# Kernel tuning notes

Measured on AMD Instinct MI355X. Metric: run time of the kernel, lower is better.

The kernel has to match this reference:

```python
import jax, jax.numpy as jnp
import numpy as np

B, N, D_ATOM, HID, L = 32, 64, 5, 256, 9
E = N * N
F_E = 2 * HID + 2  # [h_i, h_j, d^2, edge_attr]


def _gather(x, idx):
    # x: (B, N, D), idx: (B, E) -> (B, E, D)
    return jax.vmap(lambda a, i: a[i])(x, idx)


def _segsum(data, idx, n):
    # per-batch unsorted segment sum over destination node idx
    return jax.vmap(lambda d, i: jax.ops.segment_sum(d, i, num_segments=n))(data, idx)


def _safe_dist(diff):
    # sqrt of squared norm, safe at 0 (masked self-edges) for grads
    return jnp.sqrt(jnp.maximum(jnp.sum(diff ** 2, axis=-1, keepdims=True), 1e-12))


def _remove_mean(x, mask):
    n = jnp.sum(mask, axis=1, keepdims=True)
    return (x - jnp.sum(x, axis=1, keepdims=True) / n) * mask


def setup_inputs() -> dict:
    key = jax.random.key(0)
    ks = iter(jax.random.split(key, 32))

    def W(shape):
        return jax.random.normal(next(ks), shape, jnp.float32) * 0.02

    x_in = jax.random.normal(next(ks), (B, N, 3), jnp.float32)
    h_in = jax.random.uniform(next(ks), (B, N, D_ATOM), dtype=jnp.float32)
    t = jax.random.uniform(next(ks), (B, N, 1), dtype=jnp.float32)
    ii, jj = jnp.meshgrid(jnp.arange(N), jnp.arange(N), indexing='ij')
    edges = jnp.stack([ii.reshape(-1), jj.reshape(-1)], axis=-1).astype(jnp.int32)  # (E,2) all pairs
    edge_indices = jnp.broadcast_to(edges[None], (B, E, 2))
    node_mask = jnp.ones((B, N, 1), jnp.float32)
    em = (edges[:, 0] != edges[:, 1]).astype(jnp.float32)[:, None]  # mask self-edges
    edge_mask = jnp.broadcast_to(em[None], (B, E, 1))
    params = dict(
        win_w=W((D_ATOM + 1, HID)), win_b=jnp.zeros((HID,), jnp.float32),
        wout_w=W((HID, D_ATOM + 1)), wout_b=jnp.zeros((D_ATOM + 1,), jnp.float32),
        we_w1=W((L, F_E, HID)), we_b1=jnp.zeros((L, HID), jnp.float32),
        we_w2=W((L, HID, HID)), we_b2=jnp.zeros((L, HID), jnp.float32),
        attn_w=W((L, HID, 1)), attn_b=jnp.zeros((L, 1), jnp.float32),
        wh_w1=W((L, 2 * HID, HID)), wh_b1=jnp.zeros((L, HID), jnp.float32),
        wh_w2=W((L, HID, HID)), wh_b2=jnp.zeros((L, HID), jnp.float32),
        wx_w1=W((L, F_E, HID)), wx_b1=jnp.zeros((L, HID), jnp.float32),
        wx_w2=W((L, HID, HID)), wx_b2=jnp.zeros((L, HID), jnp.float32),
        wx_w3=W((L, HID, 1)),
    )
    return dict(x_in=x_in, h_in=h_in, t=t, node_mask=node_mask, edge_mask=edge_mask,
                edge_indices=edge_indices, **params)


def reference(x_in, h_in, t, node_mask, edge_mask, edge_indices,
              win_w, win_b, wout_w, wout_b,
              we_w1, we_b1, we_w2, we_b2, attn_w, attn_b,
              wh_w1, wh_b1, wh_w2, wh_b2,
              wx_w1, wx_b1, wx_w2, wx_b2, wx_w3):
    idx_i = edge_indices[..., 0]
    idx_j = edge_indices[..., 1]
    # fixed edge attribute: initial pairwise distance
    d_in = _safe_dist(_gather(x_in, idx_i) - _gather(x_in, idx_j)) * edge_mask
    h0 = jnp.concatenate([h_in, t], axis=-1) @ win_w + win_b

    def block(carry, p):
        x, h = carry
        ew1, eb1, ew2, eb2, aw, ab, hw1, hb1, hw2, hb2, xw1, xb1, xw2, xb2, xw3 = p
        diff = (_gather(x, idx_i) - _gather(x, idx_j)) * edge_mask  # (B,E,3)
        d = _safe_dist(diff)  # (B,E,1)
        feat = jnp.concatenate([_gather(h, idx_i), _gather(h, idx_j), d ** 2, d_in], axis=-1) * edge_mask
        # edge MLP + attention gate, aggregated to node i
        m = jax.nn.silu(jax.nn.silu(feat @ ew1 + eb1) @ ew2 + eb2)
        em_agg = _segsum(jax.nn.sigmoid(m @ aw + ab) * m, idx_i, N)
        h_new = (h + (jax.nn.silu(jnp.concatenate([h, em_agg], axis=-1) @ hw1 + hb1) @ hw2 + hb2)) * node_mask
        # coordinate update (no bias on last layer)
        s = jax.nn.silu(jax.nn.silu(feat @ xw1 + xb1) @ xw2 + xb2) @ xw3  # (B,E,1)
        x_new = (x + _segsum(diff / (d + 1.0) * s, idx_i, N)) * node_mask
        return (x_new, h_new), None

    stacked = (we_w1, we_b1, we_w2, we_b2, attn_w, attn_b,
               wh_w1, wh_b1, wh_w2, wh_b2, wx_w1, wx_b1, wx_w2, wx_b2, wx_w3)
    (x, h), _ = jax.lax.scan(block, (x_in, h0), stacked)
    x_out = _remove_mean((x - x_in) * node_mask, node_mask)
    h_out = ((h @ wout_w + wout_b) * node_mask)[..., :-1]
    return jnp.concatenate([x_out, h_out], axis=-1)
```

## Files before the change

### kernel.cpp

```cpp
#include <hip/hip_runtime.h>
#include <hip/hip_bf16.h>
#include <math.h>


#define NB   32
#define NN   64
#define EPB  4096
#define HID  256
#define NL   9

typedef __attribute__((ext_vector_type(8))) short bfrag;
typedef __attribute__((ext_vector_type(4))) float f32x4;
typedef __attribute__((ext_vector_type(2))) float f32x2;

__device__ __forceinline__ float fast_rcp(float x) { return __builtin_amdgcn_rcpf(x); }
__device__ __forceinline__ float silu_f(float x) { return x * fast_rcp(1.f + __expf(-x)); }
__device__ __forceinline__ float sigm_f(float x) { return fast_rcp(1.f + __expf(-x)); }
__device__ __forceinline__ ushort bf16rne(float x) {
    unsigned u = __builtin_bit_cast(unsigned, x);
    u = (u + 0x7fffu + ((u >> 16) & 1u)) >> 16;
    return (ushort)u;
}
__device__ __forceinline__ float bf16tof(ushort h) {
    unsigned u = ((unsigned)h) << 16;
    return __builtin_bit_cast(float, u);
}
__device__ __forceinline__ unsigned pk2(f32x2 v) {
    float2 f; f.x = v.x; f.y = v.y;
    __hip_bfloat162 t = __float22bfloat162_rn(f);
    unsigned u;
    __builtin_memcpy(&u, &t, 4);
    return u;
}
__device__ __forceinline__ f32x2 fma2(f32x2 a, f32x2 b, f32x2 c) {
    return __builtin_elementwise_fma(a, b, c);
}
__device__ __forceinline__ f32x4 fma4(f32x4 a, f32x4 b, f32x4 c) {
    return __builtin_elementwise_fma(a, b, c);
}
__device__ __forceinline__ f32x2 silu2(f32x2 v) {
    f32x2 e = { __expf(-v.x), __expf(-v.y) };
    f32x2 d = e + (f32x2){1.f, 1.f};
    f32x2 r = { fast_rcp(d.x), fast_rcp(d.y) };
    return v * r;
}
__device__ __forceinline__ f32x4 silu4(f32x4 v) {
    f32x4 e = { __expf(-v.x), __expf(-v.y), __expf(-v.z), __expf(-v.w) };
    f32x4 d = e + (f32x4){1.f, 1.f, 1.f, 1.f};
    f32x4 r = { fast_rcp(d.x), fast_rcp(d.y), fast_rcp(d.z), fast_rcp(d.w) };
    return v * r;
}

__global__ void edm_k0_pre(const float* __restrict__ x_in, const float* __restrict__ h_in,
                           const float* __restrict__ t_in,
                           const float* __restrict__ win_w, const float* __restrict__ win_b,
                           float* __restrict__ h0, float* __restrict__ din_ws,
                           float* __restrict__ x0)
{
    int blk = blockIdx.x, tid = threadIdx.x;
    if (blk < NB * NN) {
        int node = blk;
        float acc = win_b[tid];
        #pragma unroll
        for (int k = 0; k < 5; ++k) acc += h_in[node * 5 + k] * win_w[k * HID + tid];
        acc += t_in[node] * win_w[5 * HID + tid];
        h0[node * HID + tid] = acc;
    } else if (blk < NB * NN + 512) {
        int e = (blk - NB * NN) * 256 + tid;
        int b = e >> 12, r = e & 4095, i = r >> 6, j = r & 63;
        const float* xb = x_in + b * NN * 3;
        float d0 = xb[i*3+0] - xb[j*3+0];
        float d1 = xb[i*3+1] - xb[j*3+1];
        float d2 = xb[i*3+2] - xb[j*3+2];
        float ss = d0*d0 + d1*d1 + d2*d2;
        float d  = sqrtf(fmaxf(ss, 1e-12f));
        din_ws[e] = (i != j) ? d : 0.f;
    } else {
        int idx = (blk - (NB * NN + 512)) * 256 + tid;
        if (idx < NB * NN * 3) x0[idx] = x_in[idx];
    }
}

__global__ void edm_k5_prep(const float* __restrict__ we_w2, const float* __restrict__ wx_w2,
                            ushort* __restrict__ W2Te, ushort* __restrict__ W2Tx)
{
    __shared__ float t_s[64][65];
    int blk = blockIdx.x;
    int mat = blk / 144, rem = blk % 144, l = rem >> 4, tile = rem & 15;
    int kt = tile >> 2, nt = tile & 3;
    const float* src = (mat ? wx_w2 : we_w2) + l * HID * HID;
    ushort* dst = (mat ? W2Tx : W2Te) + l * HID * HID;
    int col = threadIdx.x & 63, rg = threadIdx.x >> 6;
    #pragma unroll
    for (int it = 0; it < 16; ++it) {
        int row = rg * 16 + it;
        t_s[row][col] = src[(kt * 64 + row) * HID + nt * 64 + col];
    }
    __syncthreads();
    #pragma unroll
    for (int it = 0; it < 16; ++it) {
        int n = rg * 16 + it;
        dst[(nt * 64 + n) * HID + kt * 64 + col] = bf16rne(t_s[col][n]);
    }
}

__global__ void edm_k5b_prep(const float* __restrict__ we_w1, const float* __restrict__ wx_w1,
                             ushort* __restrict__ W1Th, ushort* __restrict__ W1Tl)
{
    __shared__ float t_s[64][65];
    int blk = blockIdx.x;
    int tile = blk & 15, out = (blk >> 4) & 3, l = blk >> 6;
    int kt = tile >> 2, nt = tile & 3;
    const float* src = ((out >= 2) ? wx_w1 : we_w1) + l * 514 * HID + (out & 1) * 256 * HID;
    size_t doff = ((size_t)(l * 4 + out)) * HID * HID;
    ushort* dh = W1Th + doff;
    ushort* dl = W1Tl + doff;
    int col = threadIdx.x & 63, rg = threadIdx.x >> 6;
    #pragma unroll
    for (int it = 0; it < 16; ++it) {
        int row = rg * 16 + it;
        t_s[row][col] = src[(kt * 64 + row) * HID + nt * 64 + col];
    }
    __syncthreads();
    #pragma unroll
    for (int it = 0; it < 16; ++it) {
        int n = rg * 16 + it;
        float v = t_s[col][n];
        ushort h = bf16rne(v);
        float lo = v - bf16tof(h);
        dh[(nt * 64 + n) * HID + kt * 64 + col] = h;
        dl[(nt * 64 + n) * HID + kt * 64 + col] = bf16rne(lo);
    }
}

__global__ void edm_k5c_prep(const float* __restrict__ wh_w1, const float* __restrict__ wh_w2,
                             ushort* __restrict__ W3h, ushort* __restrict__ W3l,
                             ushort* __restrict__ W4h, ushort* __restrict__ W4l)
{
    __shared__ float t_s[64][65];
    int blk = blockIdx.x;
    const float* src; ushort* dh; ushort* dl; int kt, nt, Kdim;
    if (blk < 288) {
        int l = blk >> 5, tile = blk & 31;
        kt = tile >> 2; nt = tile & 3; Kdim = 512;
        src = wh_w1 + (size_t)l * 512 * HID;
        dh = W3h + (size_t)l * HID * 512;
        dl = W3l + (size_t)l * HID * 512;
    } else {
        int b2 = blk - 288;
        int l = b2 >> 4, tile = b2 & 15;
        kt = tile >> 2; nt = tile & 3; Kdim = 256;
        src = wh_w2 + (size_t)l * HID * HID;
        dh = W4h + (size_t)l * HID * HID;
        dl = W4l + (size_t)l * HID * HID;
    }
    int col = threadIdx.x & 63, rg = threadIdx.x >> 6;
    #pragma unroll
    for (int it = 0; it < 16; ++it) {
        int row = rg * 16 + it;
        t_s[row][col] = src[(size_t)(kt * 64 + row) * HID + nt * 64 + col];
    }
    __syncthreads();
    #pragma unroll
    for (int it = 0; it < 16; ++it) {
        int n = rg * 16 + it;
        float v = t_s[col][n];
        ushort h = bf16rne(v);
        float lo = v - bf16tof(h);
        dh[(size_t)(nt * 64 + n) * Kdim + kt * 64 + col] = h;
        dl[(size_t)(nt * 64 + n) * Kdim + kt * 64 + col] = bf16rne(lo);
    }
}

__global__ __launch_bounds__(256)
void edm_k1_mfma(const float* __restrict__ h,
                 const ushort* __restrict__ W1Th, const ushort* __restrict__ W1Tl,
                 const float* __restrict__ we_b1, const float* __restrict__ wx_b1,
                 const float* __restrict__ we_w2, const float* __restrict__ we_b2,
                 const float* __restrict__ attn_w, const float* __restrict__ attn_b,
                 float* __restrict__ HeA, float* __restrict__ HeB,
                 float* __restrict__ HxA, float* __restrict__ HxB,
                 float* __restrict__ self_em, int l)
{
    int tid = threadIdx.x;
    if (blockIdx.x == 512) {
        __shared__ float m1s[HID];
        __shared__ float ms[HID];
        __shared__ float wred[4];
        __shared__ float gsh;
        const float* eb1 = we_b1 + l * HID;
        m1s[tid] = silu_f(eb1[tid]);
        __syncthreads();
        const float* W2 = we_w2 + l * HID * HID;
        float acc = we_b2[l * HID + tid];
        for (int k = 0; k < HID; ++k) acc += m1s[k] * W2[k * HID + tid];
        float mv = silu_f(acc);
        ms[tid] = mv;
        float p = mv * attn_w[l * HID + tid];
        #pragma unroll
        for (int off = 32; off > 0; off >>= 1) p += __shfl_down(p, off, 64);
        if ((tid & 63) == 0) wred[tid >> 6] = p;
        __syncthreads();
        if (tid == 0) gsh = sigm_f(wred[0] + wred[1] + wred[2] + wred[3] + attn_b[l]);
        __syncthreads();
        self_em[tid] = gsh * ms[tid];
        return;
    }

    __shared__ __align__(16) ushort Ah_s[16384];
    __shared__ __align__(16) ushort Al_s[16384];

    const int cq = blockIdx.x & 3;
    const int out = (blockIdx.x >> 2) & 3;
    const int ntile = blockIdx.x >> 4;
    const int base = ntile * 64;

    {
        const int c  = tid & 31;
        const int jg = tid >> 5;
        const int k0 = c * 8;
        #pragma unroll
        for (int it = 0; it < 8; ++it) {
            int m = it * 8 + jg;
            f32x4 h0 = *(const f32x4*)&h[(base + m) * HID + k0];
            f32x4 h1 = *(const f32x4*)&h[(base + m) * HID + k0 + 4];
            uint4 phi, plo;
            {
                ushort ax = bf16rne(h0.x), ay = bf16rne(h0.y);
                phi.x = (unsigned)ax | ((unsigned)ay << 16);
                plo.x = pk2((f32x2){h0.x - bf16tof(ax), h0.y - bf16tof(ay)});
            }
            {
                ushort ax = bf16rne(h0.z), ay = bf16rne(h0.w);
                phi.y = (unsigned)ax | ((unsigned)ay << 16);
                plo.y = pk2((f32x2){h0.z - bf16tof(ax), h0.w - bf16tof(ay)});
            }
            {
                ushort ax = bf16rne(h1.x), ay = bf16rne(h1.y);
                phi.z = (unsigned)ax | ((unsigned)ay << 16);
                plo.z = pk2((f32x2){h1.x - bf16tof(ax), h1.y - bf16tof(ay)});
            }
            {
                ushort ax = bf16rne(h1.z), ay = bf16rne(h1.w);
                phi.w = (unsigned)ax | ((unsigned)ay << 16);
                plo.w = pk2((f32x2){h1.z - bf16tof(ax), h1.w - bf16tof(ay)});
            }
            unsigned off = (unsigned)(m * 256 + ((c ^ (m & 7)) * 8));
            *(uint4*)&Ah_s[off] = phi;
            *(uint4*)&Al_s[off] = plo;
        }
    }
    __syncthreads();

    const int w = tid >> 6, lane = tid & 63, quad = lane >> 4, l16 = lane & 15;
    const int col = cq * 64 + w * 16 + l16;
    const ushort* Bh = W1Th + ((size_t)(l * 4 + out)) * HID * HID + (size_t)col * HID;
    const ushort* Bl = W1Tl + ((size_t)(l * 4 + out)) * HID * HID + (size_t)col * HID;

    f32x4 acc[4];
    #pragma unroll
    for (int mt = 0; mt < 4; ++mt) acc[mt] = (f32x4){0.f, 0.f, 0.f, 0.f};

    #pragma unroll
    for (int kt = 0; kt < 8; ++kt) {
        const int kof = kt * 32 + quad * 8;
        const int ch  = (kt * 4 + quad) ^ (l16 & 7);
        bfrag bh = *(const bfrag*)&Bh[kof];
        bfrag bl = *(const bfrag*)&Bl[kof];
        bfrag ahr[4], alr[4];
        #pragma unroll
        for (int mt = 0; mt < 4; ++mt) {
            ahr[mt] = *(const bfrag*)&Ah_s[(mt * 16 + l16) * 256 + ch * 8];
            alr[mt] = *(const bfrag*)&Al_s[(mt * 16 + l16) * 256 + ch * 8];
        }
        #pragma unroll
        for (int mt = 0; mt < 4; ++mt) {
            acc[mt] = __builtin_amdgcn_mfma_f32_16x16x32_bf16(ahr[mt], bh, acc[mt], 0, 0, 0);
            acc[mt] = __builtin_amdgcn_mfma_f32_16x16x32_bf16(ahr[mt], bl, acc[mt], 0, 0, 0);
            acc[mt] = __builtin_amdgcn_mfma_f32_16x16x32_bf16(alr[mt], bh, acc[mt], 0, 0, 0);
        }
    }

    float bias = 0.f;
    if (out == 0) bias = we_b1[l * HID + col];
    else if (out == 2) bias = wx_b1[l * HID + col];
    float* dst = (out == 0) ? HeA : (out == 1) ? HeB : (out == 2) ? HxA : HxB;
    #pragma unroll
    for (int mt = 0; mt < 4; ++mt)
        #pragma unroll
        for (int r = 0; r < 4; ++r)
            dst[(base + mt * 16 + quad * 4 + r) * HID + col] = acc[mt][r] + bias;
}

__global__ __launch_bounds__(256, 4)
void edm_kb_gemm(const float* __restrict__ x_cur, float* __restrict__ x_next,
                 const float* __restrict__ HeA, const float* __restrict__ HeB,
                 const float* __restrict__ HxA, const float* __restrict__ HxB,
                 const float* __restrict__ din_ws,
                 const float* __restrict__ we_w1, const float* __restrict__ we_b1,
                 const float* __restrict__ wx_w1, const float* __restrict__ wx_b1,
                 const ushort* __restrict__ W2Te, const ushort* __restrict__ W2Tx,
                 const float* __restrict__ we_b2, const float* __restrict__ wx_b2,
                 const float* __restrict__ attn_w, const float* __restrict__ attn_b,
                 const float* __restrict__ wx_w3,
                 float* __restrict__ em_agg, int l)
{
    __shared__ __align__(16) ushort A_s[16384];
    __shared__ float red_s[256];
    __shared__ float sc_s[64];
    __shared__ float x_s[192];
    __shared__ float d2_s[64], din_s[64];

    const int tid = threadIdx.x;
    const int blk = blockIdx.x;
    const int p = blk >> 11, rem = blk & 2047;
    const int i = rem >> 5, b = rem & 31;
    const int bi = b * 64 + i;

    if (tid < 192) x_s[tid] = x_cur[b * 192 + tid];
    if (tid >= 192) {
        int j = tid - 192;
        float d0 = x_cur[b * 192 + i*3+0] - x_cur[b * 192 + j*3+0];
        float d1 = x_cur[b * 192 + i*3+1] - x_cur[b * 192 + j*3+1];
        float d2 = x_cur[b * 192 + i*3+2] - x_cur[b * 192 + j*3+2];
        float ss = d0*d0 + d1*d1 + d2*d2;
        float d  = sqrtf(fmaxf(ss, 1e-12f));
        d2_s[j]  = d * d;
        din_s[j] = din_ws[b * EPB + i * 64 + j];
    }
    __syncthreads();

    {
        const float* W1  = (p ? wx_w1 : we_w1) + l * 514 * HID;
        const float* HA  = (p ? HxA : HeA);
        const float* HB  = (p ? HxB : HeB);
        const float* b1p = (p ? wx_b1 : we_b1) + l * HID;

        const int c  = tid & 31;
        const int jg = tid >> 5;
        const int k0 = c * 8;

        f32x4 ra0 = *(const f32x4*)&HA[(b * 64 + i) * HID + k0];
        f32x4 ra1 = *(const f32x4*)&HA[(b * 64 + i) * HID + k0 + 4];
        f32x4 wa0 = *(const f32x4*)&W1[512 * HID + k0];
        f32x4 wa1 = *(const f32x4*)&W1[512 * HID + k0 + 4];
        f32x4 wb0 = *(const f32x4*)&W1[513 * HID + k0];
        f32x4 wb1 = *(const f32x4*)&W1[513 * HID + k0 + 4];
        f32x4 b10 = *(const f32x4*)&b1p[k0];
        f32x4 b11 = *(const f32x4*)&b1p[k0 + 4];
        uint4 pki;
        pki.x = pk2(silu2((f32x2){b10.x, b10.y}));
        pki.y = pk2(silu2((f32x2){b10.z, b10.w}));
        pki.z = pk2(silu2((f32x2){b11.x, b11.y}));
        pki.w = pk2(silu2((f32x2){b11.z, b11.w}));

        const float* hbp = HB + b * 64 * HID + k0;
        #pragma unroll
        for (int it = 0; it < 8; ++it) {
            int j = it * 8 + jg;
            f32x4 h0 = *(const f32x4*)&hbp[j * HID];
            f32x4 h1 = *(const f32x4*)&hbp[j * HID + 4];
            f32x2 dd = { d2_s[j], d2_s[j] };
            f32x2 dn = { din_s[j], din_s[j] };
            uint4 pkv;
            f32x2 v;
            v = fma2(dn, (f32x2){wb0.x, wb0.y},
                 fma2(dd, (f32x2){wa0.x, wa0.y},
                      (f32x2){ra0.x + h0.x, ra0.y + h0.y}));
            pkv.x = pk2(silu2(v));
            v = fma2(dn, (f32x2){wb0.z, wb0.w},
                 fma2(dd, (f32x2){wa0.z, wa0.w},
                      (f32x2){ra0.z + h0.z, ra0.w + h0.w}));
            pkv.y = pk2(silu2(v));
            v = fma2(dn, (f32x2){wb1.x, wb1.y},
                 fma2(dd, (f32x2){wa1.x, wa1.y},
                      (f32x2){ra1.x + h1.x, ra1.y + h1.y}));
            pkv.z = pk2(silu2(v));
            v = fma2(dn, (f32x2){wb1.z, wb1.w},
                 fma2(dd, (f32x2){wa1.z, wa1.w},
                      (f32x2){ra1.z + h1.z, ra1.w + h1.w}));
            pkv.w = pk2(silu2(v));
            if (j == i) pkv = pki;
            *(uint4*)&A_s[j * 256 + (unsigned)((c ^ (j & 7)) * 8)] = pkv;
        }
    }
    __syncthreads();

    const int w = tid >> 6, lane = tid & 63, quad = lane >> 4, l16 = lane & 15;
    const ushort* W2T = (p ? W2Tx : W2Te) + l * HID * HID;
    const int cb0 = w * 64 + l16;
    f32x4 acc[4][4];
    #pragma unroll
    for (int mt = 0; mt < 4; ++mt)
        #pragma unroll
        for (int nt = 0; nt < 4; ++nt) acc[mt][nt] = (f32x4){0.f, 0.f, 0.f, 0.f};

    #pragma unroll
    for (int kt = 0; kt < 8; ++kt) {
        const int kof = kt * 32 + quad * 8;
        const int ch  = (kt * 4 + quad) ^ (l16 & 7);
        bfrag bfr[4], afr[4];
        #pragma unroll
        for (int nt = 0; nt < 4; ++nt)
            bfr[nt] = *(const bfrag*)&W2T[(cb0 + nt * 16) * HID + kof];
        #pragma unroll
        for (int mt = 0; mt < 4; ++mt)
            afr[mt] = *(const bfrag*)&A_s[(mt * 16 + l16) * 256 + ch * 8];
        #pragma unroll
        for (int mt = 0; mt < 4; ++mt)
            #pragma unroll
            for (int nt = 0; nt < 4; ++nt)
                acc[mt][nt] = __builtin_amdgcn_mfma_f32_16x16x32_bf16(
                    afr[mt], bfr[nt], acc[mt][nt], 0, 0, 0);
    }

    const float* b2p = (p ? wx_b2 : we_b2) + l * HID;
    const float* vvp = p ? (wx_w3 + l * HID) : (attn_w + l * HID);
    float b2v[4], vv[4];
    #pragma unroll
    for (int nt = 0; nt < 4; ++nt) { b2v[nt] = b2p[cb0 + nt * 16]; vv[nt] = vvp[cb0 + nt * 16]; }

    #pragma unroll
    for (int mt = 0; mt < 4; ++mt)
        #pragma unroll
        for (int nt = 0; nt < 4; ++nt) {
            f32x4 bb = { b2v[nt], b2v[nt], b2v[nt], b2v[nt] };
            acc[mt][nt] = silu4(acc[mt][nt] + bb);
        }

    #pragma unroll
    for (int mt = 0; mt < 4; ++mt) {
        f32x4 t4 = acc[mt][0] * (f32x4){vv[0], vv[0], vv[0], vv[0]};
        t4 = fma4(acc[mt][1], (f32x4){vv[1], vv[1], vv[1], vv[1]}, t4);
        t4 = fma4(acc[mt][2], (f32x4){vv[2], vv[2], vv[2], vv[2]}, t4);
        t4 = fma4(acc[mt][3], (f32x4){vv[3], vv[3], vv[3], vv[3]}, t4);
        #pragma unroll
        for (int r = 0; r < 4; ++r) {
            float pd = t4[r];
            pd += __shfl_xor(pd, 1, 64); pd += __shfl_xor(pd, 2, 64);
            pd += __shfl_xor(pd, 4, 64); pd += __shfl_xor(pd, 8, 64);
            if (l16 == 0) red_s[w * 64 + mt * 16 + quad * 4 + r] = pd;
        }
    }
    __syncthreads();
    if (tid < 64) {
        float tot = red_s[tid] + red_s[64 + tid] + red_s[128 + tid] + red_s[192 + tid];
        if (p == 0) sc_s[tid] = (tid == i) ? 0.f : sigm_f(tot + attn_b[l]);
        else        sc_s[tid] = tot;
    }
    __syncthreads();

    if (p == 0) {
        f32x4 g[4];
        #pragma unroll
        for (int mt = 0; mt < 4; ++mt) g[mt] = *(const f32x4*)&sc_s[mt * 16 + quad * 4];
        #pragma unroll
        for (int nt = 0; nt < 4; ++nt) {
            f32x4 e4 = g[0] * acc[0][nt];
            e4 = fma4(g[1], acc[1][nt], e4);
            e4 = fma4(g[2], acc[2][nt], e4);
            e4 = fma4(g[3], acc[3][nt], e4);
            float e = (e4.x + e4.y) + (e4.z + e4.w);
            e += __shfl_xor(e, 16, 64); e += __shfl_xor(e, 32, 64);
            if (quad == 0) em_agg[(b * 64 + i) * HID + cb0 + nt * 16] = e;
        }
    } else {
        if (tid < 64) {
            int j = tid;
            float d0 = x_s[i*3+0] - x_s[j*3+0];
            float d1 = x_s[i*3+1] - x_s[j*3+1];
            float d2 = x_s[i*3+2] - x_s[j*3+2];
            float ss = d0*d0 + d1*d1 + d2*d2;
            float d  = sqrtf(fmaxf(ss, 1e-12f));
            float f  = fast_rcp(d + 1.f) * sc_s[j];
            float cx = d0 * f, cy = d1 * f, cz = d2 * f;
            #pragma unroll
            for (int off = 32; off > 0; off >>= 1) {
                cx += __shfl_down(cx, off, 64);
                cy += __shfl_down(cy, off, 64);
                cz += __shfl_down(cz, off, 64);
            }
            if (tid == 0) {
                x_next[bi * 3 + 0] = x_s[i*3+0] + cx;
                x_next[bi * 3 + 1] = x_s[i*3+1] + cy;
                x_next[bi * 3 + 2] = x_s[i*3+2] + cz;
            }
        }
    }
}

__global__ __launch_bounds__(256)
void edm_k3a(const float* __restrict__ h, const float* __restrict__ em_agg,
             const float* __restrict__ self_em,
             const ushort* __restrict__ W3h, const ushort* __restrict__ W3l,
             const float* __restrict__ wh_b1,
             ushort* __restrict__ Uh, ushort* __restrict__ Ul, int l)
{
    __shared__ __align__(16) ushort Ah_s[16 * 512];
    __shared__ __align__(16) ushort Al_s[16 * 512];

    const int tid = threadIdx.x;
    const int cq = blockIdx.x & 3;
    const int base = (blockIdx.x >> 2) * 16;

    {
        const int c  = tid & 63;
        const int jg = tid >> 6;
        const int k0 = c * 8;
        #pragma unroll
        for (int t = 0; t < 4; ++t) {
            int m = t * 4 + jg;
            f32x4 v0, v1;
            if (c < 32) {
                v0 = *(const f32x4*)&h[(base + m) * HID + k0];
                v1 = *(const f32x4*)&h[(base + m) * HID + k0 + 4];
            } else {
                int e0 = k0 - 256;
                f32x4 a0 = *(const f32x4*)&em_agg[(size_t)(base + m) * HID + e0];
                f32x4 a1 = *(const f32x4*)&em_agg[(size_t)(base + m) * HID + e0 + 4];
                f32x4 s0 = *(const f32x4*)&self_em[e0];
                f32x4 s1 = *(const f32x4*)&self_em[e0 + 4];
                v0 = a0 + s0; v1 = a1 + s1;
            }
            uint4 phi, plo;
            {
                ushort ax = bf16rne(v0.x), ay = bf16rne(v0.y);
                phi.x = (unsigned)ax | ((unsigned)ay << 16);
                plo.x = pk2((f32x2){v0.x - bf16tof(ax), v0.y - bf16tof(ay)});
            }
            {
                ushort ax = bf16rne(v0.z), ay = bf16rne(v0.w);
                phi.y = (unsigned)ax | ((unsigned)ay << 16);
                plo.y = pk2((f32x2){v0.z - bf16tof(ax), v0.w - bf16tof(ay)});
            }
            {
                ushort ax = bf16rne(v1.x), ay = bf16rne(v1.y);
                phi.z = (unsigned)ax | ((unsigned)ay << 16);
                plo.z = pk2((f32x2){v1.x - bf16tof(ax), v1.y - bf16tof(ay)});
            }
            {
                ushort ax = bf16rne(v1.z), ay = bf16rne(v1.w);
                phi.w = (unsigned)ax | ((unsigned)ay << 16);
                plo.w = pk2((f32x2){v1.z - bf16tof(ax), v1.w - bf16tof(ay)});
            }
            unsigned off = (unsigned)(m * 512 + ((c ^ (m & 7)) * 8));
            *(uint4*)&Ah_s[off] = phi;
            *(uint4*)&Al_s[off] = plo;
        }
    }
    __syncthreads();

    const int w = tid >> 6, lane = tid & 63, quad = lane >> 4, l16 = lane & 15;
    const int colv = cq * 64 + w * 16 + l16;

    f32x4 acc = (f32x4){0.f, 0.f, 0.f, 0.f};
    const ushort* Bh = W3h + ((size_t)l * HID + colv) * 512;
    const ushort* Bl = W3l + ((size_t)l * HID + colv) * 512;

    for (int ks = 0; ks < 16; ++ks) {
        const int kof = ks * 32 + quad * 8;
        unsigned aoff = (unsigned)(l16 * 512 + (((ks * 4 + quad) ^ (l16 & 7))) * 8);
        bfrag ah = *(const bfrag*)&Ah_s[aoff];
        bfrag al = *(const bfrag*)&Al_s[aoff];
        bfrag bh = *(const bfrag*)&Bh[kof];
        bfrag bl = *(const bfrag*)&Bl[kof];
        acc = __builtin_amdgcn_mfma_f32_16x16x32_bf16(ah, bh, acc, 0, 0, 0);
        acc = __builtin_amdgcn_mfma_f32_16x16x32_bf16(ah, bl, acc, 0, 0, 0);
        acc = __builtin_amdgcn_mfma_f32_16x16x32_bf16(al, bh, acc, 0, 0, 0);
    }

    float b1v = wh_b1[l * HID + colv];
    #pragma unroll
    for (int r = 0; r < 4; ++r) {
        float u = silu_f(acc[r] + b1v);
        ushort uh = bf16rne(u);
        float ulo = u - bf16tof(uh);
        int row = quad * 4 + r;
        size_t ao = (size_t)(base + row) * 256 + (((colv >> 3) ^ (row & 7))) * 8 + (colv & 7);
        Uh[ao] = uh;
        Ul[ao] = bf16rne(ulo);
    }
}

__global__ __launch_bounds__(256)
void edm_k3b(const float* __restrict__ h,
             const ushort* __restrict__ Uh, const ushort* __restrict__ Ul,
             const ushort* __restrict__ W4h, const ushort* __restrict__ W4l,
             const float* __restrict__ wh_b2,
             float* __restrict__ h_next, int l)
{
    const int tid = threadIdx.x;
    const int cq = blockIdx.x & 3;
    const int base = (blockIdx.x >> 2) * 16;
    const int w = tid >> 6, lane = tid & 63, quad = lane >> 4, l16 = lane & 15;
    const int colv = cq * 64 + w * 16 + l16;

    const ushort* Bh = W4h + ((size_t)l * HID + colv) * HID;
    const ushort* Bl = W4l + ((size_t)l * HID + colv) * HID;
    const ushort* Ah = Uh + (size_t)(base + l16) * 256;
    const ushort* Al = Ul + (size_t)(base + l16) * 256;

    f32x4 acc = (f32x4){0.f, 0.f, 0.f, 0.f};
    #pragma unroll
    for (int kt = 0; kt < 8; ++kt) {
        const int kof = kt * 32 + quad * 8;
        unsigned ach = (unsigned)((((kt * 4 + quad) ^ (l16 & 7))) * 8);
        bfrag ah = *(const bfrag*)&Ah[ach];
        bfrag al = *(const bfrag*)&Al[ach];
        bfrag bh = *(const bfrag*)&Bh[kof];
        bfrag bl = *(const bfrag*)&Bl[kof];
        acc = __builtin_amdgcn_mfma_f32_16x16x32_bf16(ah, bh, acc, 0, 0, 0);
        acc = __builtin_amdgcn_mfma_f32_16x16x32_bf16(ah, bl, acc, 0, 0, 0);
        acc = __builtin_amdgcn_mfma_f32_16x16x32_bf16(al, bh, acc, 0, 0, 0);
    }

    float b2v = wh_b2[l * HID + colv];
    #pragma unroll
    for (int r = 0; r < 4; ++r) {
        int node = base + quad * 4 + r;
        h_next[node * HID + colv] = h[node * HID + colv] + acc[r] + b2v;
    }
}

__global__ void edm_k4_out(const float* __restrict__ x_fin, const float* __restrict__ x_in,
                           const float* __restrict__ h_fin,
                           const float* __restrict__ wout_w, const float* __restrict__ wout_b,
                           float* __restrict__ out)
{
    __shared__ float vx[192];
    __shared__ float mean_s[3];
    int b = blockIdx.x, tid = threadIdx.x;
    if (tid < 192) vx[tid] = x_fin[b * 192 + tid] - x_in[b * 192 + tid];
    __syncthreads();
    if (tid < 3) {
        float s = 0.f;
        for (int n = 0; n < 64; ++n) s += vx[n * 3 + tid];
        mean_s[tid] = s * (1.f / 64.f);
    }
    __syncthreads();
    if (tid < 192) out[b * 512 + (tid / 3) * 8 + (tid % 3)] = vx[tid] - mean_s[tid % 3];

    int node = tid / 5, ch = tid % 5;
    float acc = wout_b[ch];
    const float* hr = h_fin + (b * 64 + node) * HID;
    for (int k = 0; k < HID; ++k) acc = fmaf(hr[k], wout_w[k * 6 + ch], acc);
    out[b * 512 + node * 8 + 3 + ch] = acc;
}

extern "C" void kernel_launch(void* const* d_in, const int* in_sizes, int n_in,
                              void* d_out, int out_size, void* d_ws, size_t ws_size,
                              hipStream_t stream)
{
    const float* x_in   = (const float*)d_in[0];
    const float* h_in   = (const float*)d_in[1];
    const float* t_in   = (const float*)d_in[2];
    const float* win_w  = (const float*)d_in[6];
    const float* win_b  = (const float*)d_in[7];
    const float* wout_w = (const float*)d_in[8];
    const float* wout_b = (const float*)d_in[9];
    const float* we_w1  = (const float*)d_in[10];
    const float* we_b1  = (const float*)d_in[11];
    const float* we_w2  = (const float*)d_in[12];
    const float* we_b2  = (const float*)d_in[13];
    const float* attn_w = (const float*)d_in[14];
    const float* attn_b = (const float*)d_in[15];
    const float* wh_w1  = (const float*)d_in[16];
    const float* wh_b1  = (const float*)d_in[17];
    const float* wh_w2  = (const float*)d_in[18];
    const float* wh_b2  = (const float*)d_in[19];
    const float* wx_w1  = (const float*)d_in[20];
    const float* wx_b1  = (const float*)d_in[21];
    const float* wx_w2  = (const float*)d_in[22];
    const float* wx_b2  = (const float*)d_in[23];
    const float* wx_w3  = (const float*)d_in[24];

    float* ws = (float*)d_ws;
    const size_t SN = (size_t)NB * NN * HID;
    float* h_a = ws;
    float* h_b = ws + SN;
    float* HeA = ws + 2 * SN;
    float* HeB = ws + 3 * SN;
    float* HxA = ws + 4 * SN;
    float* HxB = ws + 5 * SN;
    float* emg = ws + 6 * SN;
    float* din = ws + 7 * SN;
    float* x_a = din + (size_t)NB * EPB;
    float* x_b = x_a + NB * NN * 3;
    float* sem = x_b + NB * NN * 3;
    ushort* W2Te = (ushort*)(sem + 256);
    ushort* W2Tx = W2Te + (size_t)NL * HID * HID;
    ushort* W1Th = W2Tx + (size_t)NL * HID * HID;
    ushort* W1Tl = W1Th + (size_t)NL * 4 * HID * HID;
    ushort* W3h  = W1Tl + (size_t)NL * 4 * HID * HID;
    ushort* W3l  = W3h + (size_t)NL * HID * 512;
    ushort* W4h  = W3l + (size_t)NL * HID * 512;
    ushort* W4l  = W4h + (size_t)NL * HID * HID;
    ushort* Uh   = W4l + (size_t)NL * HID * HID;
    ushort* Ul   = Uh + (size_t)NB * NN * HID;

    edm_k5_prep<<<dim3(288), dim3(256), 0, stream>>>(we_w2, wx_w2, W2Te, W2Tx);
    edm_k5b_prep<<<dim3(576), dim3(256), 0, stream>>>(we_w1, wx_w1, W1Th, W1Tl);
    edm_k5c_prep<<<dim3(432), dim3(256), 0, stream>>>(wh_w1, wh_w2, W3h, W3l, W4h, W4l);

    edm_k0_pre<<<dim3(NB * NN + 512 + 24), dim3(256), 0, stream>>>(
        x_in, h_in, t_in, win_w, win_b, h_a, din, x_a);

    for (int l = 0; l < NL; ++l) {
        float* h_cur = (l & 1) ? h_b : h_a;
        float* h_nxt = (l & 1) ? h_a : h_b;
        float* x_cur = (l & 1) ? x_b : x_a;
        float* x_nxt = (l & 1) ? x_a : x_b;

        edm_k1_mfma<<<dim3(513), dim3(256), 0, stream>>>(
            h_cur, W1Th, W1Tl, we_b1, wx_b1, we_w2, we_b2, attn_w, attn_b,
            HeA, HeB, HxA, HxB, sem, l);

        edm_kb_gemm<<<dim3(2 * NB * NN), dim3(256), 0, stream>>>(
            x_cur, x_nxt, HeA, HeB, HxA, HxB, din,
            we_w1, we_b1, wx_w1, wx_b1, W2Te, W2Tx,
            we_b2, wx_b2, attn_w, attn_b, wx_w3, emg, l);

        edm_k3a<<<dim3(512), dim3(256), 0, stream>>>(
            h_cur, emg, sem, W3h, W3l, wh_b1, Uh, Ul, l);

        edm_k3b<<<dim3(512), dim3(256), 0, stream>>>(
            h_cur, Uh, Ul, W4h, W4l, wh_b2, h_nxt, l);
    }

    edm_k4_out<<<dim3(NB), dim3(320), 0, stream>>>(
        x_b, x_in, h_b, wout_w, wout_b, (float*)d_out);
}
```

Before: 1.191 ms.

## Precompute split-bf16 h in producer kernels and shrink k1 GEMM tiles

The hi/lo bf16 split and swizzle of the node features h are now written to global memory by the producers (the input embedding kernel and the k3b residual kernel). The edge-projection GEMM then reads these pre-split operands straight from global memory instead of converting h into shared memory itself. k1 also shrinks its tile from 64 to 16 rows per block, raising the grid from 513 to 2049 blocks, and drops its LDS use. The trade-off is extra global writes and reads of the split buffers, and each B fragment is now reused across fewer rows.

```diff
diff --git a/kernel.cpp b/kernel.cpp
--- a/kernel.cpp
+++ b/kernel.cpp
@@ -55,7 +55,8 @@
                            const float* __restrict__ t_in,
                            const float* __restrict__ win_w, const float* __restrict__ win_b,
                            float* __restrict__ h0, float* __restrict__ din_ws,
-                           float* __restrict__ x0)
+                           float* __restrict__ x0,
+                           ushort* __restrict__ Hh, ushort* __restrict__ Hl)
 {
     int blk = blockIdx.x, tid = threadIdx.x;
     if (blk < NB * NN) {
@@ -65,6 +66,11 @@
         for (int k = 0; k < 5; ++k) acc += h_in[node * 5 + k] * win_w[k * HID + tid];
         acc += t_in[node] * win_w[5 * HID + tid];
         h0[node * HID + tid] = acc;
+        ushort hh = bf16rne(acc);
+        float lo = acc - bf16tof(hh);
+        unsigned ao = (unsigned)(node * 256 + (((tid >> 3) ^ (node & 7)) * 8) + (tid & 7));
+        Hh[ao] = hh;
+        Hl[ao] = bf16rne(lo);
     } else if (blk < NB * NN + 512) {
         int e = (blk - NB * NN) * 256 + tid;
         int b = e >> 12, r = e & 4095, i = r >> 6, j = r & 63;
@@ -173,7 +179,7 @@
 }
 
 __global__ __launch_bounds__(256)
-void edm_k1_mfma(const float* __restrict__ h,
+void edm_k1_gemm(const ushort* __restrict__ Hh, const ushort* __restrict__ Hl,
                  const ushort* __restrict__ W1Th, const ushort* __restrict__ W1Tl,
                  const float* __restrict__ we_b1, const float* __restrict__ wx_b1,
                  const float* __restrict__ we_w2, const float* __restrict__ we_b2,
@@ -183,7 +189,7 @@
                  float* __restrict__ self_em, int l)
 {
     int tid = threadIdx.x;
-    if (blockIdx.x == 512) {
+    if (blockIdx.x == 2048) {
         __shared__ float m1s[HID];
         __shared__ float ms[HID];
         __shared__ float wred[4];
@@ -207,89 +213,38 @@
         return;
     }
 
-    __shared__ __align__(16) ushort Ah_s[16384];
-    __shared__ __align__(16) ushort Al_s[16384];
-
     const int cq = blockIdx.x & 3;
     const int out = (blockIdx.x >> 2) & 3;
-    const int ntile = blockIdx.x >> 4;
-    const int base = ntile * 64;
-
-    {
-        const int c  = tid & 31;
-        const int jg = tid >> 5;
-        const int k0 = c * 8;
-        #pragma unroll
-        for (int it = 0; it < 8; ++it) {
-            int m = it * 8 + jg;
-            f32x4 h0 = *(const f32x4*)&h[(base + m) * HID + k0];
-            f32x4 h1 = *(const f32x4*)&h[(base + m) * HID + k0 + 4];
-            uint4 phi, plo;
-            {
-                ushort ax = bf16rne(h0.x), ay = bf16rne(h0.y);
-                phi.x = (unsigned)ax | ((unsigned)ay << 16);
-                plo.x = pk2((f32x2){h0.x - bf16tof(ax), h0.y - bf16tof(ay)});
-            }
-            {
-                ushort ax = bf16rne(h0.z), ay = bf16rne(h0.w);
-                phi.y = (unsigned)ax | ((unsigned)ay << 16);
-                plo.y = pk2((f32x2){h0.z - bf16tof(ax), h0.w - bf16tof(ay)});
-            }
-            {
-                ushort ax = bf16rne(h1.x), ay = bf16rne(h1.y);
-                phi.z = (unsigned)ax | ((unsigned)ay << 16);
-                plo.z = pk2((f32x2){h1.x - bf16tof(ax), h1.y - bf16tof(ay)});
-            }
-            {
-                ushort ax = bf16rne(h1.z), ay = bf16rne(h1.w);
-                phi.w = (unsigned)ax | ((unsigned)ay << 16);
-                plo.w = pk2((f32x2){h1.z - bf16tof(ax), h1.w - bf16tof(ay)});
-            }
-            unsigned off = (unsigned)(m * 256 + ((c ^ (m & 7)) * 8));
-            *(uint4*)&Ah_s[off] = phi;
-            *(uint4*)&Al_s[off] = plo;
-        }
-    }
-    __syncthreads();
-
+    const int base = (blockIdx.x >> 4) * 16;
     const int w = tid >> 6, lane = tid & 63, quad = lane >> 4, l16 = lane & 15;
-    const int col = cq * 64 + w * 16 + l16;
-    const ushort* Bh = W1Th + ((size_t)(l * 4 + out)) * HID * HID + (size_t)col * HID;
-    const ushort* Bl = W1Tl + ((size_t)(l * 4 + out)) * HID * HID + (size_t)col * HID;
-
-    f32x4 acc[4];
-    #pragma unroll
-    for (int mt = 0; mt < 4; ++mt) acc[mt] = (f32x4){0.f, 0.f, 0.f, 0.f};
-
+    const int colv = cq * 64 + w * 16 + l16;
+
+    const ushort* Bh = W1Th + ((size_t)(l * 4 + out)) * HID * HID + (size_t)colv * HID;
+    const ushort* Bl = W1Tl + ((size_t)(l * 4 + out)) * HID * HID + (size_t)colv * HID;
+    const ushort* Ah = Hh + (size_t)(base + l16) * 256;
+    const ushort* Al = Hl + (size_t)(base + l16) * 256;
+
+    f32x4 acc = (f32x4){0.f, 0.f, 0.f, 0.f};
     #pragma unroll
     for (int kt = 0; kt < 8; ++kt) {
         const int kof = kt * 32 + quad * 8;
-        const int ch  = (kt * 4 + quad) ^ (l16 & 7);
+        unsigned ach = (unsigned)((((kt * 4 + quad) ^ (l16 & 7))) * 8);
+        bfrag ah = *(const bfrag*)&Ah[ach];
+        bfrag al = *(const bfrag*)&Al[ach];
         bfrag bh = *(const bfrag*)&Bh[kof];
         bfrag bl = *(const bfrag*)&Bl[kof];
-        bfrag ahr[4], alr[4];
-        #pragma unroll
-        for (int mt = 0; mt < 4; ++mt) {
-            ahr[mt] = *(const bfrag*)&Ah_s[(mt * 16 + l16) * 256 + ch * 8];
-            alr[mt] = *(const bfrag*)&Al_s[(mt * 16 + l16) * 256 + ch * 8];
-        }
-        #pragma unroll
-        for (int mt = 0; mt < 4; ++mt) {
-            acc[mt] = __builtin_amdgcn_mfma_f32_16x16x32_bf16(ahr[mt], bh, acc[mt], 0, 0, 0);
-            acc[mt] = __builtin_amdgcn_mfma_f32_16x16x32_bf16(ahr[mt], bl, acc[mt], 0, 0, 0);
-            acc[mt] = __builtin_amdgcn_mfma_f32_16x16x32_bf16(alr[mt], bh, acc[mt], 0, 0, 0);
-        }
+        acc = __builtin_amdgcn_mfma_f32_16x16x32_bf16(ah, bh, acc, 0, 0, 0);
+        acc = __builtin_amdgcn_mfma_f32_16x16x32_bf16(ah, bl, acc, 0, 0, 0);
+        acc = __builtin_amdgcn_mfma_f32_16x16x32_bf16(al, bh, acc, 0, 0, 0);
     }
 
     float bias = 0.f;
-    if (out == 0) bias = we_b1[l * HID + col];
-    else if (out == 2) bias = wx_b1[l * HID + col];
+    if (out == 0) bias = we_b1[l * HID + colv];
+    else if (out == 2) bias = wx_b1[l * HID + colv];
     float* dst = (out == 0) ? HeA : (out == 1) ? HeB : (out == 2) ? HxA : HxB;
     #pragma unroll
-    for (int mt = 0; mt < 4; ++mt)
-        #pragma unroll
-        for (int r = 0; r < 4; ++r)
-            dst[(base + mt * 16 + quad * 4 + r) * HID + col] = acc[mt][r] + bias;
+    for (int r = 0; r < 4; ++r)
+        dst[(base + quad * 4 + r) * HID + colv] = acc[r] + bias;
 }
 
 __global__ __launch_bounds__(256, 4)
@@ -587,7 +542,8 @@
              const ushort* __restrict__ Uh, const ushort* __restrict__ Ul,
              const ushort* __restrict__ W4h, const ushort* __restrict__ W4l,
              const float* __restrict__ wh_b2,
-             float* __restrict__ h_next, int l)
+             float* __restrict__ h_next,
+             ushort* __restrict__ Hh, ushort* __restrict__ Hl, int l)
 {
     const int tid = threadIdx.x;
     const int cq = blockIdx.x & 3;
@@ -618,7 +574,13 @@
     #pragma unroll
     for (int r = 0; r < 4; ++r) {
         int node = base + quad * 4 + r;
-        h_next[node * HID + colv] = h[node * HID + colv] + acc[r] + b2v;
+        float hn = h[node * HID + colv] + acc[r] + b2v;
+        h_next[node * HID + colv] = hn;
+        ushort hh = bf16rne(hn);
+        float lo = hn - bf16tof(hh);
+        size_t ao = (size_t)node * 256 + (((colv >> 3) ^ (node & 7))) * 8 + (colv & 7);
+        Hh[ao] = hh;
+        Hl[ao] = bf16rne(lo);
     }
 }
 
@@ -697,13 +659,15 @@
     ushort* W4l  = W4h + (size_t)NL * HID * HID;
     ushort* Uh   = W4l + (size_t)NL * HID * HID;
     ushort* Ul   = Uh + (size_t)NB * NN * HID;
+    ushort* Hh   = Ul + (size_t)NB * NN * HID;
+    ushort* Hl   = Hh + (size_t)NB * NN * HID;
 
     edm_k5_prep<<<dim3(288), dim3(256), 0, stream>>>(we_w2, wx_w2, W2Te, W2Tx);
     edm_k5b_prep<<<dim3(576), dim3(256), 0, stream>>>(we_w1, wx_w1, W1Th, W1Tl);
     edm_k5c_prep<<<dim3(432), dim3(256), 0, stream>>>(wh_w1, wh_w2, W3h, W3l, W4h, W4l);
 
     edm_k0_pre<<<dim3(NB * NN + 512 + 24), dim3(256), 0, stream>>>(
-        x_in, h_in, t_in, win_w, win_b, h_a, din, x_a);
+        x_in, h_in, t_in, win_w, win_b, h_a, din, x_a, Hh, Hl);
 
     for (int l = 0; l < NL; ++l) {
         float* h_cur = (l & 1) ? h_b : h_a;
@@ -711,8 +675,8 @@
         float* x_cur = (l & 1) ? x_b : x_a;
         float* x_nxt = (l & 1) ? x_a : x_b;
 
-        edm_k1_mfma<<<dim3(513), dim3(256), 0, stream>>>(
-            h_cur, W1Th, W1Tl, we_b1, wx_b1, we_w2, we_b2, attn_w, attn_b,
+        edm_k1_gemm<<<dim3(2049), dim3(256), 0, stream>>>(
+            Hh, Hl, W1Th, W1Tl, we_b1, wx_b1, we_w2, we_b2, attn_w, attn_b,
             HeA, HeB, HxA, HxB, sem, l);
 
         edm_kb_gemm<<<dim3(2 * NB * NN), dim3(256), 0, stream>>>(
@@ -724,7 +688,7 @@
             h_cur, emg, sem, W3h, W3l, wh_b1, Uh, Ul, l);
 
         edm_k3b<<<dim3(512), dim3(256), 0, stream>>>(
-            h_cur, Uh, Ul, W4h, W4l, wh_b2, h_nxt, l);
+            h_cur, Uh, Ul, W4h, W4l, wh_b2, h_nxt, Hh, Hl, l);
     }
 
     edm_k4_out<<<dim3(NB), dim3(320), 0, stream>>>(
```

After: 1.303 ms. 9.4% more time.
